# Performance work log

Measured on AMD Instinct MI355X. Metric: run time of the kernel, lower is better.

The kernel has to match this reference:

```python
import jax, jax.numpy as jnp
import numpy as np

NH = 2            # num heads
B = 2             # batch
CH = (64, 128, 256, 512)
HW = (128, 64, 32, 16)


def _mha(q, kv, w_in, b_in, w_out, b_out):
    # q, kv: [B, C, H, W] feature maps; seq layout (L, B, C) as in torch MHA (batch_first=False)
    Bq, C, H, W = q.shape
    L = H * W
    S = kv.shape[2] * kv.shape[3]
    qs = q.reshape(Bq, C, L).transpose(2, 0, 1)    # [L,B,C]
    ks = kv.reshape(Bq, C, S).transpose(2, 0, 1)   # [S,B,C]
    wq, wk, wv = jnp.split(w_in, 3, axis=0)        # torch in_proj_weight rows = [q; k; v]
    bq, bk, bv = jnp.split(b_in, 3)
    dh = C // NH
    qp = (qs @ wq.T + bq).reshape(L, Bq, NH, dh)
    kp = (ks @ wk.T + bk).reshape(S, Bq, NH, dh)
    vp = (ks @ wv.T + bv).reshape(S, Bq, NH, dh)
    scale = 1.0 / jnp.sqrt(jnp.asarray(dh, qp.dtype))
    scores = jnp.einsum('lbhd,sbhd->bhls', qp * scale, kp)  # [B,H,L,S]
    attn = jax.nn.softmax(scores, axis=-1)
    out = jnp.einsum('bhls,sbhd->lbhd', attn, vp).reshape(L, Bq, C)
    out = out @ w_out.T + b_out                    # out_proj
    return out.transpose(1, 2, 0).reshape(Bq, C, H, W)


def _level(fx1, fx2, fx3, w12, b12, ow12, ob12, w13, b13, ow13, ob13, sqw, sqb):
    att1 = _mha(fx1, fx2, w12, b12, ow12, ob12)
    att2 = _mha(fx1, fx3, w13, b13, ow13, ob13)
    cat = jnp.concatenate([fx1, att1, att2], axis=1)          # [B, 3C, H, W]
    return jnp.einsum('oc,bchw->bohw', sqw, cat) + sqb[None, :, None, None]  # 1x1 conv


def setup_inputs() -> dict:
    key = jax.random.key(0)
    ks = iter(jax.random.split(key, 64))
    d = {}
    for lvl in range(4):
        c, s = CH[lvl], HW[lvl]
        d[f'f1_{lvl}'] = jax.random.normal(next(ks), (B, c, s, s), jnp.float32)
    for lvl in range(1, 4):
        c, s = CH[lvl], HW[lvl]
        d[f'f2_{lvl}'] = jax.random.normal(next(ks), (B, c, s, s), jnp.float32)
        d[f'f3_{lvl}'] = jax.random.normal(next(ks), (B, c, s, s), jnp.float32)
    for i in (1, 2, 3):
        c = CH[i]
        sc = 1.0 / np.sqrt(c).astype(np.float32)
        for p in ('a12', 'a13'):
            d[f'{p}w{i}'] = jax.random.normal(next(ks), (3 * c, c), jnp.float32) * sc
            d[f'{p}b{i}'] = jnp.zeros((3 * c,), jnp.float32)
            d[f'{p}ow{i}'] = jax.random.normal(next(ks), (c, c), jnp.float32) * sc
            d[f'{p}ob{i}'] = jnp.zeros((c,), jnp.float32)
        d[f'sqw{i}'] = jax.random.normal(next(ks), (c, 3 * c), jnp.float32) * np.float32(1.0 / np.sqrt(3 * c))
        d[f'sqb{i}'] = jnp.zeros((c,), jnp.float32)
    return d


def reference(f1_0, f1_1, f1_2, f1_3, f2_1, f2_2, f2_3, f3_1, f3_2, f3_3,
              a12w1, a12b1, a12ow1, a12ob1, a13w1, a13b1, a13ow1, a13ob1, sqw1, sqb1,
              a12w2, a12b2, a12ow2, a12ob2, a13w2, a13b2, a13ow2, a13ob2, sqw2, sqb2,
              a12w3, a12b3, a12ow3, a12ob3, a13w3, a13b3, a13ow3, a13ob3, sqw3, sqb3):
    out0 = f1_0  # level 0 passes through untouched
    out1 = _level(f1_1, f2_1, f3_1, a12w1, a12b1, a12ow1, a12ob1, a13w1, a13b1, a13ow1, a13ob1, sqw1, sqb1)
    out2 = _level(f1_2, f2_2, f3_2, a12w2, a12b2, a12ow2, a12ob2, a13w2, a13b2, a13ow2, a13ob2, sqw2, sqb2)
    out3 = _level(f1_3, f2_3, f3_3, a12w3, a12b3, a12ow3, a12ob3, a13w3, a13b3, a13ow3, a13ob3, sqw3, sqb3)
    return (out0, out1, out2, out3)
```

## Files before the change

### kernel.cpp

```cpp
#include <hip/hip_runtime.h>
#include <hip/hip_bf16.h>
#include <math.h>

#define NHEADS 2

typedef unsigned short u16;
typedef __attribute__((ext_vector_type(8))) unsigned short u16x8;
typedef __attribute__((ext_vector_type(4))) unsigned short u16x4;
typedef __attribute__((ext_vector_type(8))) short short8;
typedef __attribute__((ext_vector_type(4))) short short4v;
typedef __attribute__((ext_vector_type(4))) float f32x4;

__device__ __forceinline__ u16 f2bf(float x) {
    __hip_bfloat16 h = __float2bfloat16(x);
    return __builtin_bit_cast(unsigned short, h);
}

__global__ __launch_bounds__(256) void gemm_qkv(
    const float* __restrict__ f1, const float* __restrict__ f2,
    const float* __restrict__ f3,
    const float* __restrict__ w12, const float* __restrict__ b12,
    const float* __restrict__ w13, const float* __restrict__ b13,
    u16* __restrict__ Qa, u16* __restrict__ Ka, u16* __restrict__ Va,
    u16* __restrict__ Qb, u16* __restrict__ Kb, u16* __restrict__ Vb,
    int M, int C, int L, int dh, float qscale, int gx, int perAtt)
{
    const int att = blockIdx.x / perAtt;
    const int r = blockIdx.x - att * perAtt;
    const int n0 = (r % gx) * 64;
    const int m0 = (r / gx) * 64;
    const int K = C;
    __shared__ __align__(16) u16 Xs[64][72];
    __shared__ __align__(16) u16 Ws[64][72];
    const int tid = threadIdx.x;
    const int wid = tid >> 6, lane = tid & 63;
    const int lo = lane & 15, hi = lane >> 4;
    const int wm = wid >> 1, wn = wid & 1;

    const float* __restrict__ Xf = (n0 < C) ? f1 : (att ? f3 : f2);
    const float* __restrict__ W = att ? w13 : w12;
    const float* __restrict__ bias = att ? b13 : b12;
    const int bb = m0 / L;
    const int l0 = m0 - bb * L;

    f32x4 acc[2][2];
    #pragma unroll
    for (int i = 0; i < 2; ++i)
        #pragma unroll
        for (int j = 0; j < 2; ++j)
            #pragma unroll
            for (int rr = 0; rr < 4; ++rr) acc[i][j][rr] = 0.f;

    f32x4 xregf[4];
    f32x4 wreg[4];
    const int kx = tid >> 4;
    const int lc = tid & 15;

    auto load_x = [&](int k0) {
        #pragma unroll
        for (int i = 0; i < 4; ++i)
            xregf[i] = *(const f32x4*)&Xf[((size_t)(bb * C) + k0 + kx + 16 * i) * L + l0 + lc * 4];
    };
    auto store_x = [&]() {
        #pragma unroll
        for (int i = 0; i < 4; ++i)
            #pragma unroll
            for (int j = 0; j < 4; ++j)
                Xs[lc * 4 + j][kx + 16 * i] = f2bf(xregf[i][j]);
    };
    auto load_w = [&](int k0) {
        #pragma unroll
        for (int p = 0; p < 4; ++p) {
            int c = tid + p * 256;
            int row = c >> 4, kc = c & 15;
            wreg[p] = *(const f32x4*)&W[(size_t)(n0 + row) * K + k0 + kc * 4];
        }
    };

    load_x(0);
    load_w(0);
    const int ns = K / 64;
    for (int s = 0; s < ns; ++s) {
        __syncthreads();
        store_x();
        #pragma unroll
        for (int p = 0; p < 4; ++p) {
            int c = tid + p * 256;
            int row = c >> 4, kc = c & 15;
            u16x4 cv = {f2bf(wreg[p][0]), f2bf(wreg[p][1]),
                        f2bf(wreg[p][2]), f2bf(wreg[p][3])};
            *(u16x4*)&Ws[row][kc * 4] = cv;
        }
        __syncthreads();
        if (s + 1 < ns) { load_x((s + 1) * 64); load_w((s + 1) * 64); }
        #pragma unroll
        for (int kk = 0; kk < 2; ++kk) {
            short8 wf0 = *(const short8*)&Ws[wn * 32 + lo][kk * 32 + hi * 8];
            short8 wf1 = *(const short8*)&Ws[wn * 32 + 16 + lo][kk * 32 + hi * 8];
            short8 xf0 = *(const short8*)&Xs[wm * 32 + lo][kk * 32 + hi * 8];
            short8 xf1 = *(const short8*)&Xs[wm * 32 + 16 + lo][kk * 32 + hi * 8];
            acc[0][0] = __builtin_amdgcn_mfma_f32_16x16x32_bf16(wf0, xf0, acc[0][0], 0, 0, 0);
            acc[0][1] = __builtin_amdgcn_mfma_f32_16x16x32_bf16(wf1, xf0, acc[0][1], 0, 0, 0);
            acc[1][0] = __builtin_amdgcn_mfma_f32_16x16x32_bf16(wf0, xf1, acc[1][0], 0, 0, 0);
            acc[1][1] = __builtin_amdgcn_mfma_f32_16x16x32_bf16(wf1, xf1, acc[1][1], 0, 0, 0);
        }
    }

    #pragma unroll
    for (int nt = 0; nt < 2; ++nt) {
        const int nb = n0 + wn * 32 + nt * 16 + hi * 4;
        const float b0 = bias[nb + 0], b1 = bias[nb + 1];
        const float b2 = bias[nb + 2], b3 = bias[nb + 3];
        const int which = nb / C;
        const int co = nb - which * C;
        const int h = co / dh;
        const int dd = co - h * dh;
        u16* dst = (which == 0) ? (att ? Qb : Qa)
                 : (which == 1) ? (att ? Kb : Ka) : (att ? Vb : Va);
        const float sc = (which == 0) ? qscale : 1.0f;
        #pragma unroll
        for (int mt = 0; mt < 2; ++mt) {
            int m = m0 + wm * 32 + mt * 16 + lo;
            int b_ = m / L; int l = m - b_ * L;
            u16x4 pk = {f2bf((acc[mt][nt][0] + b0) * sc),
                        f2bf((acc[mt][nt][1] + b1) * sc),
                        f2bf((acc[mt][nt][2] + b2) * sc),
                        f2bf((acc[mt][nt][3] + b3) * sc)};
            *(u16x4*)&dst[((size_t)(b_ * NHEADS + h) * L + l) * dh + dd] = pk;
        }
    }
}

__global__ __launch_bounds__(256) void prep_w(
    const float* __restrict__ s1, const float* __restrict__ oa1,
    const float* __restrict__ ob1, float* __restrict__ w1,
    const float* __restrict__ s2, const float* __restrict__ oa2,
    const float* __restrict__ ob2, float* __restrict__ w2,
    const float* __restrict__ s3, const float* __restrict__ oa3,
    const float* __restrict__ ob3, float* __restrict__ w3)
{
    int bid = blockIdx.x;
    int C; const float *sqw, *owa, *owb; float* wp;
    if (bid < 12)      { C = 128; sqw = s1; owa = oa1; owb = ob1; wp = w1; }
    else if (bid < 60) { bid -= 12; C = 256; sqw = s2; owa = oa2; owb = ob2; wp = w2; }
    else               { bid -= 60; C = 512; sqw = s3; owa = oa3; owb = ob3; wp = w3; }
    const int K3 = 3 * C;
    const int gxw = K3 / 64;
    const int n0 = (bid / gxw) * 64;
    const int kc0 = (bid % gxw) * 64;
    const int tid = threadIdx.x;

    if (kc0 < C) {
        for (int p = tid; p < 64 * 64; p += 256) {
            int i = p >> 6, j = p & 63;
            wp[(size_t)(n0 + i) * K3 + kc0 + j] = sqw[(size_t)(n0 + i) * K3 + kc0 + j];
        }
        return;
    }
    const int which = kc0 / C;
    const int kp0 = kc0 - which * C;
    const float* __restrict__ ow = (which == 1) ? owa : owb;

    __shared__ __align__(16) u16 As[64][72];
    __shared__ __align__(16) u16 Bs[64][72];
    const int wid = tid >> 6, lane = tid & 63;
    const int lo = lane & 15, hi = lane >> 4;
    const int wm = wid >> 1, wn = wid & 1;

    f32x4 acc[2][2];
    #pragma unroll
    for (int i = 0; i < 2; ++i)
        #pragma unroll
        for (int j = 0; j < 2; ++j)
            #pragma unroll
            for (int rr = 0; rr < 4; ++rr) acc[i][j][rr] = 0.f;

    for (int ct = 0; ct < C / 64; ++ct) {
        __syncthreads();
        for (int p = tid; p < 64 * 64; p += 256) {
            int i = p >> 6, j = p & 63;
            As[i][j] = f2bf(sqw[(size_t)(n0 + i) * K3 + which * C + ct * 64 + j]);
            Bs[j][i] = f2bf(ow[(size_t)(ct * 64 + i) * C + kp0 + j]);
        }
        __syncthreads();
        #pragma unroll
        for (int kk = 0; kk < 2; ++kk) {
            short8 wf0 = *(const short8*)&As[wn * 32 + lo][kk * 32 + hi * 8];
            short8 wf1 = *(const short8*)&As[wn * 32 + 16 + lo][kk * 32 + hi * 8];
            short8 xf0 = *(const short8*)&Bs[wm * 32 + lo][kk * 32 + hi * 8];
            short8 xf1 = *(const short8*)&Bs[wm * 32 + 16 + lo][kk * 32 + hi * 8];
            acc[0][0] = __builtin_amdgcn_mfma_f32_16x16x32_bf16(wf0, xf0, acc[0][0], 0, 0, 0);
            acc[0][1] = __builtin_amdgcn_mfma_f32_16x16x32_bf16(wf1, xf0, acc[0][1], 0, 0, 0);
            acc[1][0] = __builtin_amdgcn_mfma_f32_16x16x32_bf16(wf0, xf1, acc[1][0], 0, 0, 0);
            acc[1][1] = __builtin_amdgcn_mfma_f32_16x16x32_bf16(wf1, xf1, acc[1][1], 0, 0, 0);
        }
    }
    #pragma unroll
    for (int nt = 0; nt < 2; ++nt) {
        const int nb = n0 + wn * 32 + nt * 16 + hi * 4;
        #pragma unroll
        for (int mt = 0; mt < 2; ++mt) {
            const int col = kc0 + wm * 32 + mt * 16 + lo;
            #pragma unroll
            for (int rr = 0; rr < 4; ++rr)
                wp[(size_t)(nb + rr) * K3 + col] = acc[mt][nt][rr];
        }
    }
}

__global__ __launch_bounds__(256) void prep_b(
    const float* __restrict__ s1, const float* __restrict__ oba1,
    const float* __restrict__ obb1, const float* __restrict__ sqb1, float* __restrict__ b1,
    const float* __restrict__ s2, const float* __restrict__ oba2,
    const float* __restrict__ obb2, const float* __restrict__ sqb2, float* __restrict__ b2,
    const float* __restrict__ s3, const float* __restrict__ oba3,
    const float* __restrict__ obb3, const float* __restrict__ sqb3, float* __restrict__ b3)
{
    int bid = blockIdx.x;
    int C, n;
    const float *sqw, *oba, *obb, *sqb; float* bp;
    if (bid < 128)      { C = 128; n = bid;       sqw = s1; oba = oba1; obb = obb1; sqb = sqb1; bp = b1; }
    else if (bid < 384) { C = 256; n = bid - 128; sqw = s2; oba = oba2; obb = obb2; sqb = sqb2; bp = b2; }
    else                { C = 512; n = bid - 384; sqw = s3; oba = oba3; obb = obb3; sqb = sqb3; bp = b3; }

    const float* row = sqw + (size_t)n * 3 * C;
    float s = 0.f;
    for (int c = threadIdx.x; c < C; c += 256)
        s += row[C + c] * oba[c] + row[2 * C + c] * obb[c];
    #pragma unroll
    for (int off = 1; off < 64; off <<= 1)
        s += __shfl_xor(s, off);
    __shared__ float ws[4];
    const int wv = threadIdx.x >> 6;
    if ((threadIdx.x & 63) == 0) ws[wv] = s;
    __syncthreads();
    if (threadIdx.x == 0)
        bp[n] = sqb[n] + ws[0] + ws[1] + ws[2] + ws[3];
}

__global__ __launch_bounds__(256) void gemm_squeeze(
    const float* __restrict__ F1, const u16* __restrict__ X1,
    const u16* __restrict__ X2,
    const float* __restrict__ W, const float* __restrict__ bias,
    float* __restrict__ out, int M, int C, int L)
{
    const int n0 = blockIdx.x * 64;
    const int m0 = blockIdx.y * 64;
    const int K = 3 * C;
    __shared__ __align__(16) u16 Xs[64][72];
    __shared__ __align__(16) u16 Ws[64][72];
    const int tid = threadIdx.x;
    const int wid = tid >> 6, lane = tid & 63;
    const int lo = lane & 15, hi = lane >> 4;
    const int wm = wid >> 1, wn = wid & 1;
    const int bb = m0 / L;
    const int l0 = m0 - bb * L;

    f32x4 acc[2][2];
    #pragma unroll
    for (int i = 0; i < 2; ++i)
        #pragma unroll
        for (int j = 0; j < 2; ++j)
            #pragma unroll
            for (int rr = 0; rr < 4; ++rr) acc[i][j][rr] = 0.f;

    f32x4 xregf[4];
    u16x8 xreg[2];
    f32x4 wreg[4];
    const int kx = tid >> 4;
    const int lc = tid & 15;

    auto load_x = [&](int k0) {
        if (k0 < C) {
            #pragma unroll
            for (int i = 0; i < 4; ++i)
                xregf[i] = *(const f32x4*)&F1[((size_t)(bb * C) + k0 + kx + 16 * i) * L + l0 + lc * 4];
        } else {
            const u16* src = (k0 < 2 * C) ? X1 : X2;
            int kl = k0 - ((k0 < 2 * C) ? C : 2 * C);
            #pragma unroll
            for (int p = 0; p < 2; ++p) {
                int c = tid + p * 256;
                int row = c >> 3, kc = c & 7;
                xreg[p] = *(const u16x8*)&src[(size_t)(m0 + row) * C + kl + kc * 8];
            }
        }
    };
    auto store_x = [&](int k0) {
        if (k0 < C) {
            #pragma unroll
            for (int i = 0; i < 4; ++i)
                #pragma unroll
                for (int j = 0; j < 4; ++j)
                    Xs[lc * 4 + j][kx + 16 * i] = f2bf(xregf[i][j]);
        } else {
            #pragma unroll
            for (int p = 0; p < 2; ++p) {
                int c = tid + p * 256;
                int row = c >> 3, kc = c & 7;
                *(u16x8*)&Xs[row][kc * 8] = xreg[p];
            }
        }
    };
    auto load_w = [&](int k0) {
        #pragma unroll
        for (int p = 0; p < 4; ++p) {
            int c = tid + p * 256;
            int row = c >> 4, kc = c & 15;
            wreg[p] = *(const f32x4*)&W[(size_t)(n0 + row) * K + k0 + kc * 4];
        }
    };

    load_x(0);
    load_w(0);
    const int ns = K / 64;
    for (int s = 0; s < ns; ++s) {
        __syncthreads();
        store_x(s * 64);
        #pragma unroll
        for (int p = 0; p < 4; ++p) {
            int c = tid + p * 256;
            int row = c >> 4, kc = c & 15;
            u16x4 cv = {f2bf(wreg[p][0]), f2bf(wreg[p][1]),
                        f2bf(wreg[p][2]), f2bf(wreg[p][3])};
            *(u16x4*)&Ws[row][kc * 4] = cv;
        }
        __syncthreads();
        if (s + 1 < ns) { load_x((s + 1) * 64); load_w((s + 1) * 64); }
        #pragma unroll
        for (int kk = 0; kk < 2; ++kk) {
            short8 wf0 = *(const short8*)&Ws[wn * 32 + lo][kk * 32 + hi * 8];
            short8 wf1 = *(const short8*)&Ws[wn * 32 + 16 + lo][kk * 32 + hi * 8];
            short8 xf0 = *(const short8*)&Xs[wm * 32 + lo][kk * 32 + hi * 8];
            short8 xf1 = *(const short8*)&Xs[wm * 32 + 16 + lo][kk * 32 + hi * 8];
            acc[0][0] = __builtin_amdgcn_mfma_f32_16x16x32_bf16(wf0, xf0, acc[0][0], 0, 0, 0);
            acc[0][1] = __builtin_amdgcn_mfma_f32_16x16x32_bf16(wf1, xf0, acc[0][1], 0, 0, 0);
            acc[1][0] = __builtin_amdgcn_mfma_f32_16x16x32_bf16(wf0, xf1, acc[1][0], 0, 0, 0);
            acc[1][1] = __builtin_amdgcn_mfma_f32_16x16x32_bf16(wf1, xf1, acc[1][1], 0, 0, 0);
        }
    }

    #pragma unroll
    for (int nt = 0; nt < 2; ++nt) {
        const int nb = n0 + wn * 32 + nt * 16 + hi * 4;
        const float b0 = bias[nb + 0], b1 = bias[nb + 1];
        const float b2 = bias[nb + 2], b3 = bias[nb + 3];
        #pragma unroll
        for (int mt = 0; mt < 2; ++mt) {
            int m = m0 + wm * 32 + mt * 16 + lo;
            int b_ = m / L; int l = m - b_ * L;
            out[((size_t)(b_ * C + nb + 0)) * L + l] = acc[mt][nt][0] + b0;
            out[((size_t)(b_ * C + nb + 1)) * L + l] = acc[mt][nt][1] + b1;
            out[((size_t)(b_ * C + nb + 2)) * L + l] = acc[mt][nt][2] + b2;
            out[((size_t)(b_ * C + nb + 3)) * L + l] = acc[mt][nt][3] + b3;
        }
    }
}

template <int DH, int NPAR, int NQS>
__global__ __launch_bounds__(128 * NPAR) void flash_split(
    const u16* __restrict__ Q1, const u16* __restrict__ K1,
    const u16* __restrict__ V1, u16* __restrict__ O1,
    const u16* __restrict__ Q2, const u16* __restrict__ K2,
    const u16* __restrict__ V2, u16* __restrict__ O2, int L, int S)
{
    constexpr int KB = 64;
    constexpr int QW = 16 * NQS;
    constexpr int QB = 2 * QW;
    constexpr int NKK = DH / 32;
    constexpr int NNT = DH / 16;
    constexpr int DG = DH / 8;
    constexpr int SLOTS = DG / 8;
    constexpr int SZ_VT = 2 * NPAR * DH * KB * 2;
    constexpr int MST = DH + 4;
    constexpr int P = NPAR - 1;

    __shared__ __align__(16) char smem[SZ_VT];
    u16 (*Vt)[NPAR][DH][KB] = (u16 (*)[NPAR][DH][KB])smem;
    float* MrgAcc = (float*)smem;
    float* MrgML  = (float*)(smem + (size_t)2 * P * QW * MST * 4);

    const int nQT = L / QB;
    const int perAtt = 2 * NHEADS * nQT;
    const int att = blockIdx.x / perAtt;
    const int rem = blockIdx.x - att * perAtt;
    const int qt = rem % nQT;
    const int bh = rem / nQT;
    const u16* __restrict__ Q = att ? Q2 : Q1;
    const u16* __restrict__ K = att ? K2 : K1;
    const u16* __restrict__ V = att ? V2 : V1;
    u16* __restrict__ O = att ? O2 : O1;

    const int tid = threadIdx.x;
    const int w = tid >> 6;
    const int lane = tid & 63;
    const int lo = lane & 15, hi = lane >> 4;
    const int qg = w & 1, par = w >> 1;
    const int q0 = qt * QB + qg * QW;

    short8 qf[NQS][NKK];
    #pragma unroll
    for (int qs = 0; qs < NQS; ++qs)
        #pragma unroll
        for (int kk = 0; kk < NKK; ++kk)
            qf[qs][kk] = *(const short8*)&Q[((size_t)bh * L + q0 + qs * 16 + lo) * DH + kk * 32 + hi * 8];

    f32x4 acc[NQS][NNT];
    #pragma unroll
    for (int qs = 0; qs < NQS; ++qs)
        #pragma unroll
        for (int nt = 0; nt < NNT; ++nt)
            #pragma unroll
            for (int r = 0; r < 4; ++r) acc[qs][nt][r] = 0.f;
    float m_i[NQS], l_i[NQS];
    #pragma unroll
    for (int qs = 0; qs < NQS; ++qs) { m_i[qs] = -1e30f; l_i[qs] = 0.f; }

    const u16* Kbase = K + (size_t)bh * S * DH;
    const u16* Vbase = V + (size_t)bh * S * DH;

    short8 kf[4][NKK];
    auto load_kf = [&](int r) {
        const u16* Kt = Kbase + (size_t)(NPAR * r + par) * KB * DH;
        #pragma unroll
        for (int st = 0; st < 4; ++st)
            #pragma unroll
            for (int kk = 0; kk < NKK; ++kk)
                kf[st][kk] = *(const short8*)&Kt[(size_t)(st * 16 + lo) * DH + kk * 32 + hi * 8];
    };

    const int pt = tid >> 7;
    const int u = tid & 127;
    int dV0[SLOTS], sV0[SLOTS];
    #pragma unroll
    for (int z = 0; z < SLOTS; ++z) {
        int e = u + z * 128;
        dV0[z] = (e % DG) * 8;
        sV0[z] = (e / DG) * 4;
    }

    u16x8 vreg[SLOTS][4];

    auto loadslots = [&](int r) {
        const u16* Vp = Vbase + (size_t)(NPAR * r + pt) * KB * DH;
        #pragma unroll
        for (int z = 0; z < SLOTS; ++z)
            #pragma unroll
            for (int si = 0; si < 4; ++si)
                vreg[z][si] = *(const u16x8*)&Vp[(size_t)(sV0[z] + si) * DH + dV0[z]];
    };
    auto writeslots = [&](int buf) {
        #pragma unroll
        for (int z = 0; z < SLOTS; ++z)
            #pragma unroll
            for (int j = 0; j < 8; ++j) {
                int d = dV0[z] + j;
                int g = ((d >> 3) ^ d) & 7;
                int scol = (sV0[z] & 7) | ((((sV0[z] >> 3) ^ g) & 7) << 3);
                u16x4 wj = {vreg[z][0][j], vreg[z][1][j], vreg[z][2][j], vreg[z][3][j]};
                *(u16x4*)&Vt[buf][pt][d][scol] = wj;
            }
    };

    const int NR = S / (KB * NPAR);

    load_kf(0);
    loadslots(0);
    writeslots(0);
    __syncthreads();
    if (1 < NR) loadslots(1);

    for (int r = 0; r < NR; ++r) {
        const int cur = r & 1;

        f32x4 sacc[4][NQS];
        #pragma unroll
        for (int st = 0; st < 4; ++st)
            #pragma unroll
            for (int qs = 0; qs < NQS; ++qs)
                #pragma unroll
                for (int rr = 0; rr < 4; ++rr) sacc[st][qs][rr] = 0.f;
        #pragma unroll
        for (int st = 0; st < 4; ++st) {
            #pragma unroll
            for (int kk = 0; kk < NKK; ++kk) {
                #pragma unroll
                for (int qs = 0; qs < NQS; ++qs)
                    sacc[st][qs] = __builtin_amdgcn_mfma_f32_16x16x32_bf16(
                        kf[st][kk], qf[qs][kk], sacc[st][qs], 0, 0, 0);
            }
        }

        if (r + 1 < NR) load_kf(r + 1);

        float mn[NQS], ts[NQS];
        #pragma unroll
        for (int qs = 0; qs < NQS; ++qs) {
            float tm = -1e30f;
            #pragma unroll
            for (int st = 0; st < 4; ++st)
                #pragma unroll
                for (int rr = 0; rr < 4; ++rr) tm = fmaxf(tm, sacc[st][qs][rr]);
            tm = fmaxf(tm, __shfl_xor(tm, 16));
            tm = fmaxf(tm, __shfl_xor(tm, 32));
            const bool grow = __any(tm > m_i[qs] + 8.0f);
            mn[qs] = grow ? fmaxf(m_i[qs], tm) : m_i[qs];
            ts[qs] = 0.f;
            if (grow) {
                float alpha = __builtin_amdgcn_exp2f(m_i[qs] - mn[qs]);
                m_i[qs] = mn[qs];
                l_i[qs] *= alpha;
                float ar[4];
                #pragma unroll
                for (int rr = 0; rr < 4; ++rr) ar[rr] = __shfl(alpha, hi * 4 + rr);
                #pragma unroll
                for (int nt = 0; nt < NNT; ++nt)
                    #pragma unroll
                    for (int rr = 0; rr < 4; ++rr) acc[qs][nt][rr] *= ar[rr];
            }
        }

        if (r + 1 < NR) writeslots(cur ^ 1);

        __builtin_amdgcn_s_setprio(1);
        #pragma unroll
        for (int st = 0; st < 4; ++st) {
            short4v pa_[NQS];
            #pragma unroll
            for (int qs = 0; qs < NQS; ++qs) {
                float p0 = __builtin_amdgcn_exp2f(sacc[st][qs][0] - mn[qs]);
                float p1 = __builtin_amdgcn_exp2f(sacc[st][qs][1] - mn[qs]);
                float p2 = __builtin_amdgcn_exp2f(sacc[st][qs][2] - mn[qs]);
                float p3 = __builtin_amdgcn_exp2f(sacc[st][qs][3] - mn[qs]);
                ts[qs] += (p0 + p1) + (p2 + p3);
                short4v pk = {(short)f2bf(p0), (short)f2bf(p1),
                              (short)f2bf(p2), (short)f2bf(p3)};
                pa_[qs] = pk;
            }
            const int s0 = st * 16 + hi * 4;
            #pragma unroll
            for (int nt = 0; nt < NNT; ++nt) {
                int d = nt * 16 + lo;
                int g = ((d >> 3) ^ d) & 7;
                int scol = (s0 & 7) | ((((s0 >> 3) ^ g) & 7) << 3);
                short4v vb = *(const short4v*)&Vt[cur][par][d][scol];
                #pragma unroll
                for (int qs = 0; qs < NQS; ++qs)
                    acc[qs][nt] = __builtin_amdgcn_mfma_f32_16x16x16bf16_1k(
                        pa_[qs], vb, acc[qs][nt], 0, 0, 0);
            }
        }
        __builtin_amdgcn_s_setprio(0);

        #pragma unroll
        for (int qs = 0; qs < NQS; ++qs) {
            float t2 = ts[qs];
            t2 += __shfl_xor(t2, 16);
            t2 += __shfl_xor(t2, 32);
            l_i[qs] += t2;
        }

        __syncthreads();
        if (r + 2 < NR) loadslots(r + 2);
    }

    const int b_ = bh / NHEADS, h_ = bh % NHEADS;
    if (par != 0) {
        const int mi = qg * P + par - 1;
        float* ma = MrgAcc + (size_t)mi * QW * MST;
        #pragma unroll
        for (int qs = 0; qs < NQS; ++qs) {
            #pragma unroll
            for (int nt = 0; nt < NNT; ++nt)
                #pragma unroll
                for (int rr = 0; rr < 4; ++rr)
                    ma[(size_t)(qs * 16 + hi * 4 + rr) * MST + nt * 16 + lo] = acc[qs][nt][rr];
            if (hi == 0) {
                MrgML[(mi * 2 + 0) * QW + qs * 16 + lo] = m_i[qs];
                MrgML[(mi * 2 + 1) * QW + qs * 16 + lo] = l_i[qs];
            }
        }
    }
    __syncthreads();
    if (par == 0) {
        #pragma unroll
        for (int qs = 0; qs < NQS; ++qs) {
            float mp[P > 0 ? P : 1], lp[P > 0 ? P : 1];
            float mt = m_i[qs];
            #pragma unroll
            for (int p = 0; p < P; ++p) {
                mp[p] = MrgML[((qg * P + p) * 2 + 0) * QW + qs * 16 + lo];
                lp[p] = MrgML[((qg * P + p) * 2 + 1) * QW + qs * 16 + lo];
                mt = fmaxf(mt, mp[p]);
            }
            float c0 = __builtin_amdgcn_exp2f(m_i[qs] - mt);
            float lt = c0 * l_i[qs];
            float cp[P > 0 ? P : 1];
            #pragma unroll
            for (int p = 0; p < P; ++p) {
                cp[p] = __builtin_amdgcn_exp2f(mp[p] - mt);
                lt += cp[p] * lp[p];
            }
            float linv = 1.0f / lt;
            c0 *= linv;
            #pragma unroll
            for (int p = 0; p < P; ++p) cp[p] *= linv;
            float c0r[4], cpr[P > 0 ? P : 1][4];
            #pragma unroll
            for (int rr = 0; rr < 4; ++rr) {
                c0r[rr] = __shfl(c0, hi * 4 + rr);
                #pragma unroll
                for (int p = 0; p < P; ++p) cpr[p][rr] = __shfl(cp[p], hi * 4 + rr);
            }
            #pragma unroll
            for (int nt = 0; nt < NNT; ++nt)
                #pragma unroll
                for (int rr = 0; rr < 4; ++rr) {
                    int q = qs * 16 + hi * 4 + rr;
                    float ov = acc[qs][nt][rr] * c0r[rr];
                    #pragma unroll
                    for (int p = 0; p < P; ++p)
                        ov += MrgAcc[((size_t)(qg * P + p) * QW + q) * MST + nt * 16 + lo] * cpr[p][rr];
                    O[(((size_t)b_ * L + q0 + q) * NHEADS + h_) * DH + nt * 16 + lo] = f2bf(ov);
                }
        }
    }
}

template <int DH, int NQS, int PRE>
__global__ __launch_bounds__(128) void flash_mfma(
    const u16* __restrict__ Q1, const u16* __restrict__ K1,
    const u16* __restrict__ V1, u16* __restrict__ O1,
    const u16* __restrict__ Q2, const u16* __restrict__ K2,
    const u16* __restrict__ V2, u16* __restrict__ O2, int L, int S)
{
    constexpr int KB = 64;
    constexpr int QW = NQS * 16;
    constexpr int QB = 2 * QW;
    constexpr int DH8 = DH / 8;
    constexpr int KC = (KB * DH8) / 128;
    constexpr int VU = (16 * DH8) / 128;
    constexpr int NKK = DH / 32;
    constexpr int NNT = DH / 16;

    __shared__ __align__(16) u16 Ks[KB][DH + 8];
    __shared__ __align__(16) u16 Vt[DH][KB];

    const int nQT = L / QB;
    const int perAtt = 2 * NHEADS * nQT;
    const int att = blockIdx.x / perAtt;
    const int rem = blockIdx.x - att * perAtt;
    const int qt = rem % nQT;
    const int bh = rem / nQT;
    const u16* __restrict__ Q = att ? Q2 : Q1;
    const u16* __restrict__ K = att ? K2 : K1;
    const u16* __restrict__ V = att ? V2 : V1;
    u16* __restrict__ O = att ? O2 : O1;

    const int tid = threadIdx.x;
    const int wv = tid >> 6;
    const int lane = tid & 63;
    const int lo = lane & 15;
    const int hi = lane >> 4;
    const int q0 = qt * QB + wv * QW;

    short8 qf[NQS][NKK];
    #pragma unroll
    for (int qs = 0; qs < NQS; ++qs)
        #pragma unroll
        for (int kk = 0; kk < NKK; ++kk)
            qf[qs][kk] = *(const short8*)&Q[((size_t)bh * L + q0 + qs * 16 + lo) * DH + kk * 32 + hi * 8];

    f32x4 acc[NQS][NNT];
    #pragma unroll
    for (int qs = 0; qs < NQS; ++qs)
        #pragma unroll
        for (int nt = 0; nt < NNT; ++nt)
            #pragma unroll
            for (int r = 0; r < 4; ++r) acc[qs][nt][r] = 0.f;
    float m_i[NQS], l_i[NQS];
    #pragma unroll
    for (int qs = 0; qs < NQS; ++qs) { m_i[qs] = -1e30f; l_i[qs] = 0.f; }

    const int NT = S / KB;
    u16x8 kreg[PRE ? KC : 1];
    u16x8 vreg[PRE ? VU : 1][4];

    const u16* Kbase = K + (size_t)bh * S * DH;
    const u16* Vbase = V + (size_t)bh * S * DH;

    auto vwrite = [&](int d, int s0, u16x4 wj) {
        int g = ((d >> 3) ^ d) & 7;
        int scol = (s0 & 7) | ((((s0 >> 3) ^ g) & 7) << 3);
        *(u16x4*)&Vt[d][scol] = wj;
    };

    if (PRE) {
        #pragma unroll
        for (int i = 0; i < KC; ++i) {
            int idx = tid + i * 128;
            kreg[i] = *(const u16x8*)&Kbase[(size_t)(idx / DH8) * DH + (idx % DH8) * 8];
        }
        #pragma unroll
        for (int u = 0; u < VU; ++u) {
            int uu = tid + u * 128;
            int d0 = (uu % DH8) * 8, s0 = (uu / DH8) * 4;
            #pragma unroll
            for (int si = 0; si < 4; ++si)
                vreg[u][si] = *(const u16x8*)&Vbase[(size_t)(s0 + si) * DH + d0];
        }
    }

    for (int t = 0; t < NT; ++t) {
        __syncthreads();
        if (PRE) {
            #pragma unroll
            for (int i = 0; i < KC; ++i) {
                int idx = tid + i * 128;
                *(u16x8*)&Ks[idx / DH8][(idx % DH8) * 8] = kreg[i];
            }
            #pragma unroll
            for (int u = 0; u < VU; ++u) {
                int uu = tid + u * 128;
                int d0 = (uu % DH8) * 8, s0 = (uu / DH8) * 4;
                #pragma unroll
                for (int j = 0; j < 8; ++j) {
                    u16x4 wj = {vreg[u][0][j], vreg[u][1][j], vreg[u][2][j], vreg[u][3][j]};
                    vwrite(d0 + j, s0, wj);
                }
            }
        } else {
            const u16* Kp = Kbase + (size_t)t * KB * DH;
            const u16* Vp = Vbase + (size_t)t * KB * DH;
            #pragma unroll
            for (int i = 0; i < KC; ++i) {
                int idx = tid + i * 128;
                *(u16x8*)&Ks[idx / DH8][(idx % DH8) * 8] =
                    *(const u16x8*)&Kp[(size_t)(idx / DH8) * DH + (idx % DH8) * 8];
            }
            #pragma unroll
            for (int u = 0; u < VU; ++u) {
                int uu = tid + u * 128;
                int d0 = (uu % DH8) * 8, s0 = (uu / DH8) * 4;
                u16x8 v0 = *(const u16x8*)&Vp[(size_t)(s0 + 0) * DH + d0];
                u16x8 v1 = *(const u16x8*)&Vp[(size_t)(s0 + 1) * DH + d0];
                u16x8 v2 = *(const u16x8*)&Vp[(size_t)(s0 + 2) * DH + d0];
                u16x8 v3 = *(const u16x8*)&Vp[(size_t)(s0 + 3) * DH + d0];
                #pragma unroll
                for (int j = 0; j < 8; ++j) {
                    u16x4 wj = {v0[j], v1[j], v2[j], v3[j]};
                    vwrite(d0 + j, s0, wj);
                }
            }
        }
        __syncthreads();

        if (PRE && t + 1 < NT) {
            const u16* Kp = Kbase + (size_t)(t + 1) * KB * DH;
            const u16* Vp = Vbase + (size_t)(t + 1) * KB * DH;
            #pragma unroll
            for (int i = 0; i < KC; ++i) {
                int idx = tid + i * 128;
                kreg[i] = *(const u16x8*)&Kp[(size_t)(idx / DH8) * DH + (idx % DH8) * 8];
            }
            #pragma unroll
            for (int u = 0; u < VU; ++u) {
                int uu = tid + u * 128;
                int d0 = (uu % DH8) * 8, s0 = (uu / DH8) * 4;
                #pragma unroll
                for (int si = 0; si < 4; ++si)
                    vreg[u][si] = *(const u16x8*)&Vp[(size_t)(s0 + si) * DH + d0];
            }
        }

        f32x4 sacc[4][NQS];
        #pragma unroll
        for (int st = 0; st < 4; ++st)
            #pragma unroll
            for (int qs = 0; qs < NQS; ++qs)
                #pragma unroll
                for (int r = 0; r < 4; ++r) sacc[st][qs][r] = 0.f;
        #pragma unroll
        for (int st = 0; st < 4; ++st) {
            #pragma unroll
            for (int kk = 0; kk < NKK; ++kk) {
                short8 a = *(const short8*)&Ks[st * 16 + lo][kk * 32 + hi * 8];
                #pragma unroll
                for (int qs = 0; qs < NQS; ++qs)
                    sacc[st][qs] = __builtin_amdgcn_mfma_f32_16x16x32_bf16(
                        a, qf[qs][kk], sacc[st][qs], 0, 0, 0);
            }
        }

        float mn[NQS], ts[NQS];
        #pragma unroll
        for (int qs = 0; qs < NQS; ++qs) {
            float tm = -1e30f;
            #pragma unroll
            for (int st = 0; st < 4; ++st)
                #pragma unroll
                for (int r = 0; r < 4; ++r) tm = fmaxf(tm, sacc[st][qs][r]);
            tm = fmaxf(tm, __shfl_xor(tm, 16));
            tm = fmaxf(tm, __shfl_xor(tm, 32));
            const bool grow = __any(tm > m_i[qs] + 8.0f);
            mn[qs] = grow ? fmaxf(m_i[qs], tm) : m_i[qs];
            ts[qs] = 0.f;
            if (grow) {
                float alpha = __builtin_amdgcn_exp2f(m_i[qs] - mn[qs]);
                m_i[qs] = mn[qs];
                l_i[qs] *= alpha;
                float ar[4];
                #pragma unroll
                for (int r = 0; r < 4; ++r) ar[r] = __shfl(alpha, hi * 4 + r);
                #pragma unroll
                for (int nt = 0; nt < NNT; ++nt)
                    #pragma unroll
                    for (int r = 0; r < 4; ++r) acc[qs][nt][r] *= ar[r];
            }
        }

        #pragma unroll
        for (int st = 0; st < 4; ++st) {
            short4v pa_[NQS];
            #pragma unroll
            for (int qs = 0; qs < NQS; ++qs) {
                float p0 = __builtin_amdgcn_exp2f(sacc[st][qs][0] - mn[qs]);
                float p1 = __builtin_amdgcn_exp2f(sacc[st][qs][1] - mn[qs]);
                float p2 = __builtin_amdgcn_exp2f(sacc[st][qs][2] - mn[qs]);
                float p3 = __builtin_amdgcn_exp2f(sacc[st][qs][3] - mn[qs]);
                ts[qs] += (p0 + p1) + (p2 + p3);
                short4v pk = {(short)f2bf(p0), (short)f2bf(p1),
                              (short)f2bf(p2), (short)f2bf(p3)};
                pa_[qs] = pk;
            }
            const int s0 = st * 16 + hi * 4;
            #pragma unroll
            for (int nt = 0; nt < NNT; ++nt) {
                int d = nt * 16 + lo;
                int g = ((d >> 3) ^ d) & 7;
                int scol = (s0 & 7) | ((((s0 >> 3) ^ g) & 7) << 3);
                short4v vb = *(const short4v*)&Vt[d][scol];
                #pragma unroll
                for (int qs = 0; qs < NQS; ++qs)
                    acc[qs][nt] = __builtin_amdgcn_mfma_f32_16x16x16bf16_1k(
                        pa_[qs], vb, acc[qs][nt], 0, 0, 0);
            }
        }

        #pragma unroll
        for (int qs = 0; qs < NQS; ++qs) {
            float t2 = ts[qs];
            t2 += __shfl_xor(t2, 16);
            t2 += __shfl_xor(t2, 32);
            l_i[qs] += t2;
        }
    }

    const int b_ = bh / NHEADS, h_ = bh % NHEADS;
    #pragma unroll
    for (int qs = 0; qs < NQS; ++qs) {
        float inv = 1.0f / l_i[qs];
        float ir[4];
        #pragma unroll
        for (int r = 0; r < 4; ++r) ir[r] = __shfl(inv, hi * 4 + r);
        #pragma unroll
        for (int nt = 0; nt < NNT; ++nt)
            #pragma unroll
            for (int r = 0; r < 4; ++r) {
                int l = q0 + qs * 16 + hi * 4 + r;
                O[(((size_t)b_ * L + l) * NHEADS + h_) * DH + nt * 16 + lo] =
                    f2bf(acc[qs][nt][r] * ir[r]);
            }
    }
}


extern "C" void kernel_launch(void* const* d_in, const int* in_sizes, int n_in,
                              void* d_out, int out_size, void* d_ws, size_t ws_size,
                              hipStream_t stream)
{
    static const int CHs[4] = {64, 128, 256, 512};
    static const int HWs[4] = {128, 64, 32, 16};

    const float* f1[4] = {(const float*)d_in[0], (const float*)d_in[1],
                          (const float*)d_in[2], (const float*)d_in[3]};
    const float* f2[4] = {nullptr, (const float*)d_in[4], (const float*)d_in[6],
                          (const float*)d_in[8]};
    const float* f3[4] = {nullptr, (const float*)d_in[5], (const float*)d_in[7],
                          (const float*)d_in[9]};

    size_t out0_elems = (size_t)in_sizes[0];
    hipMemcpyAsync(d_out, d_in[0], out0_elems * sizeof(float),
                   hipMemcpyDeviceToDevice, stream);

    const size_t SL = (size_t)2 * 4096 * 128;
    u16* wsu = (u16*)d_ws;
    u16* Qa  = wsu + 0 * SL;
    u16* Ka  = wsu + 1 * SL;
    u16* Va  = wsu + 2 * SL;
    u16* Qb  = wsu + 3 * SL;
    u16* Kb  = wsu + 4 * SL;
    u16* Vb  = wsu + 5 * SL;
    u16* Ana = wsu + 6 * SL;
    u16* Anb = wsu + 7 * SL;
    float* wp1 = (float*)(wsu + 8 * SL);
    float* wp2 = wp1 + (size_t)128 * 384;
    float* wp3 = wp2 + (size_t)256 * 768;
    float* bp1 = wp3 + (size_t)512 * 1536;
    float* bp2 = bp1 + 512;
    float* bp3 = bp2 + 512;

    const float* SQW[3]; const float* OWA[3]; const float* OWB[3];
    const float* OBA[3]; const float* OBB[3]; const float* SQB[3];
    for (int l = 0; l < 3; ++l) {
        const int bi = 10 + l * 10;
        OWA[l] = (const float*)d_in[bi + 2];
        OBA[l] = (const float*)d_in[bi + 3];
        OWB[l] = (const float*)d_in[bi + 6];
        OBB[l] = (const float*)d_in[bi + 7];
        SQW[l] = (const float*)d_in[bi + 8];
        SQB[l] = (const float*)d_in[bi + 9];
    }

    prep_w<<<252, 256, 0, stream>>>(SQW[0], OWA[0], OWB[0], wp1,
                                    SQW[1], OWA[1], OWB[1], wp2,
                                    SQW[2], OWA[2], OWB[2], wp3);
    prep_b<<<896, 256, 0, stream>>>(SQW[0], OBA[0], OBB[0], SQB[0], bp1,
                                    SQW[1], OBA[1], OBB[1], SQB[1], bp2,
                                    SQW[2], OBA[2], OBB[2], SQB[2], bp3);

    const float LOG2E = 1.44269504088896340736f;

    size_t outOff = out0_elems;
    for (int lvl = 1; lvl <= 3; ++lvl) {
        const int C = CHs[lvl];
        const int Hs = HWs[lvl];
        const int L = Hs * Hs;
        const int dh = C / NHEADS;
        const int M = 2 * L;
        const float qscale = LOG2E / sqrtf((float)dh);
        const int bi = 10 + (lvl - 1) * 10;
        const float* a12w = (const float*)d_in[bi + 0];
        const float* a12b = (const float*)d_in[bi + 1];
        const float* a13w = (const float*)d_in[bi + 4];
        const float* a13b = (const float*)d_in[bi + 5];
        float* wp = (lvl == 1) ? wp1 : (lvl == 2) ? wp2 : wp3;
        float* bp = (lvl == 1) ? bp1 : (lvl == 2) ? bp2 : bp3;

        const int gx = 3 * C / 64;
        const int perAtt = gx * (M / 64);
        gemm_qkv<<<2 * perAtt, 256, 0, stream>>>(
            f1[lvl], f2[lvl], f3[lvl], a12w, a12b, a13w, a13b,
            Qa, Ka, Va, Qb, Kb, Vb, M, C, L, dh, qscale, gx, perAtt);

        if (dh == 64)
            flash_split<64, 4, 2><<<2 * (2 * NHEADS) * (L / 64), 512, 0, stream>>>(
                Qa, Ka, Va, Ana, Qb, Kb, Vb, Anb, L, L);
        else if (dh == 128)
            flash_split<128, 2, 1><<<2 * (2 * NHEADS) * (L / 32), 256, 0, stream>>>(
                Qa, Ka, Va, Ana, Qb, Kb, Vb, Anb, L, L);
        else
            flash_mfma<256, 1, 0><<<2 * (2 * NHEADS) * (L / 32), 128, 0, stream>>>(
                Qa, Ka, Va, Ana, Qb, Kb, Vb, Anb, L, L);

        dim3 gsq(C / 64, M / 64);
        gemm_squeeze<<<gsq, 256, 0, stream>>>(f1[lvl], Ana, Anb, wp, bp,
                                              (float*)d_out + outOff, M, C, L);
        outOff += (size_t)2 * C * L;
    }
}
```

Baseline: 280.6 us.

## Merge per-level QKV, prep, and squeeze launches into batched multi-level kernels

Gives each level its own Q/K/V/attention workspace slices so the three levels no longer share buffers. That allows all QKV projections plus the weight and bias prep to run in one launch, and all three squeeze GEMMs in another. This cuts the launch count, removes serialization between levels, and fills the GPU better on the small levels. The cost is a larger workspace footprint and branchy dispatch inside the merged kernels, which may raise register pressure.

```diff
diff --git a/kernel.cpp b/kernel.cpp
--- a/kernel.cpp
+++ b/kernel.cpp
@@ -16,30 +16,40 @@
     return __builtin_bit_cast(unsigned short, h);
 }
 
-__global__ __launch_bounds__(256) void gemm_qkv(
-    const float* __restrict__ f1, const float* __restrict__ f2,
-    const float* __restrict__ f3,
-    const float* __restrict__ w12, const float* __restrict__ b12,
-    const float* __restrict__ w13, const float* __restrict__ b13,
-    u16* __restrict__ Qa, u16* __restrict__ Ka, u16* __restrict__ Va,
-    u16* __restrict__ Qb, u16* __restrict__ Kb, u16* __restrict__ Vb,
-    int M, int C, int L, int dh, float qscale, int gx, int perAtt)
+struct QkvLvl {
+    const float *f1, *f2, *f3;
+    const float *w12, *b12, *w13, *b13;
+    u16 *Qa, *Ka, *Va, *Qb, *Kb, *Vb;
+    int C, L, dh, gx, perAtt;
+    float qscale;
+};
+struct PrepArgs {
+    const float *sqw[3], *owa[3], *owb[3], *oba[3], *obb[3], *sqb[3];
+    float *wp[3], *bp[3];
+};
+struct SqLvl {
+    const float* F1; const u16 *X1, *X2;
+    const float *W, *bias; float* out;
+    int M, C, L, gx, nblk;
+};
+
+__device__ __forceinline__ void qkv_dev(const QkvLvl& A, int lbid,
+                                        u16 (*Xs)[72], u16 (*Ws)[72])
 {
-    const int att = blockIdx.x / perAtt;
-    const int r = blockIdx.x - att * perAtt;
-    const int n0 = (r % gx) * 64;
-    const int m0 = (r / gx) * 64;
+    const int att = lbid / A.perAtt;
+    const int r = lbid - att * A.perAtt;
+    const int n0 = (r % A.gx) * 64;
+    const int m0 = (r / A.gx) * 64;
+    const int C = A.C, L = A.L, dh = A.dh;
     const int K = C;
-    __shared__ __align__(16) u16 Xs[64][72];
-    __shared__ __align__(16) u16 Ws[64][72];
     const int tid = threadIdx.x;
     const int wid = tid >> 6, lane = tid & 63;
     const int lo = lane & 15, hi = lane >> 4;
     const int wm = wid >> 1, wn = wid & 1;
 
-    const float* __restrict__ Xf = (n0 < C) ? f1 : (att ? f3 : f2);
-    const float* __restrict__ W = att ? w13 : w12;
-    const float* __restrict__ bias = att ? b13 : b12;
+    const float* __restrict__ Xf = (n0 < C) ? A.f1 : (att ? A.f3 : A.f2);
+    const float* __restrict__ W = att ? A.w13 : A.w12;
+    const float* __restrict__ bias = att ? A.b13 : A.b12;
     const int bb = m0 / L;
     const int l0 = m0 - bb * L;
 
@@ -115,9 +125,9 @@
         const int co = nb - which * C;
         const int h = co / dh;
         const int dd = co - h * dh;
-        u16* dst = (which == 0) ? (att ? Qb : Qa)
-                 : (which == 1) ? (att ? Kb : Ka) : (att ? Vb : Va);
-        const float sc = (which == 0) ? qscale : 1.0f;
+        u16* dst = (which == 0) ? (att ? A.Qb : A.Qa)
+                 : (which == 1) ? (att ? A.Kb : A.Ka) : (att ? A.Vb : A.Va);
+        const float sc = (which == 0) ? A.qscale : 1.0f;
         #pragma unroll
         for (int mt = 0; mt < 2; ++mt) {
             int m = m0 + wm * 32 + mt * 16 + lo;
@@ -131,19 +141,17 @@
     }
 }
 
-__global__ __launch_bounds__(256) void prep_w(
-    const float* __restrict__ s1, const float* __restrict__ oa1,
-    const float* __restrict__ ob1, float* __restrict__ w1,
-    const float* __restrict__ s2, const float* __restrict__ oa2,
-    const float* __restrict__ ob2, float* __restrict__ w2,
-    const float* __restrict__ s3, const float* __restrict__ oa3,
-    const float* __restrict__ ob3, float* __restrict__ w3)
+__device__ __forceinline__ void prepw_dev(const PrepArgs& P, int bid,
+                                          u16 (*As)[72], u16 (*Bs)[72])
 {
-    int bid = blockIdx.x;
-    int C; const float *sqw, *owa, *owb; float* wp;
-    if (bid < 12)      { C = 128; sqw = s1; owa = oa1; owb = ob1; wp = w1; }
-    else if (bid < 60) { bid -= 12; C = 256; sqw = s2; owa = oa2; owb = ob2; wp = w2; }
-    else               { bid -= 60; C = 512; sqw = s3; owa = oa3; owb = ob3; wp = w3; }
+    int C; int lv;
+    if (bid < 12)      { C = 128; lv = 0; }
+    else if (bid < 60) { bid -= 12; C = 256; lv = 1; }
+    else               { bid -= 60; C = 512; lv = 2; }
+    const float* sqw = P.sqw[lv];
+    const float* owa = P.owa[lv];
+    const float* owb = P.owb[lv];
+    float* wp = P.wp[lv];
     const int K3 = 3 * C;
     const int gxw = K3 / 64;
     const int n0 = (bid / gxw) * 64;
@@ -161,8 +169,6 @@
     const int kp0 = kc0 - which * C;
     const float* __restrict__ ow = (which == 1) ? owa : owb;
 
-    __shared__ __align__(16) u16 As[64][72];
-    __shared__ __align__(16) u16 Bs[64][72];
     const int wid = tid >> 6, lane = tid & 63;
     const int lo = lane & 15, hi = lane >> 4;
     const int wm = wid >> 1, wn = wid & 1;
@@ -208,20 +214,17 @@
     }
 }
 
-__global__ __launch_bounds__(256) void prep_b(
-    const float* __restrict__ s1, const float* __restrict__ oba1,
-    const float* __restrict__ obb1, const float* __restrict__ sqb1, float* __restrict__ b1,
-    const float* __restrict__ s2, const float* __restrict__ oba2,
-    const float* __restrict__ obb2, const float* __restrict__ sqb2, float* __restrict__ b2,
-    const float* __restrict__ s3, const float* __restrict__ oba3,
-    const float* __restrict__ obb3, const float* __restrict__ sqb3, float* __restrict__ b3)
+__device__ __forceinline__ void prepb_dev(const PrepArgs& P, int bid, float* ws4)
 {
-    int bid = blockIdx.x;
-    int C, n;
-    const float *sqw, *oba, *obb, *sqb; float* bp;
-    if (bid < 128)      { C = 128; n = bid;       sqw = s1; oba = oba1; obb = obb1; sqb = sqb1; bp = b1; }
-    else if (bid < 384) { C = 256; n = bid - 128; sqw = s2; oba = oba2; obb = obb2; sqb = sqb2; bp = b2; }
-    else                { C = 512; n = bid - 384; sqw = s3; oba = oba3; obb = obb3; sqb = sqb3; bp = b3; }
+    int C, n, lv;
+    if (bid < 128)      { C = 128; n = bid;       lv = 0; }
+    else if (bid < 384) { C = 256; n = bid - 128; lv = 1; }
+    else                { C = 512; n = bid - 384; lv = 2; }
+    const float* sqw = P.sqw[lv];
+    const float* oba = P.oba[lv];
+    const float* obb = P.obb[lv];
+    const float* sqb = P.sqb[lv];
+    float* bp = P.bp[lv];
 
     const float* row = sqw + (size_t)n * 3 * C;
     float s = 0.f;
@@ -230,25 +233,39 @@
     #pragma unroll
     for (int off = 1; off < 64; off <<= 1)
         s += __shfl_xor(s, off);
-    __shared__ float ws[4];
     const int wv = threadIdx.x >> 6;
-    if ((threadIdx.x & 63) == 0) ws[wv] = s;
+    if ((threadIdx.x & 63) == 0) ws4[wv] = s;
     __syncthreads();
     if (threadIdx.x == 0)
-        bp[n] = sqb[n] + ws[0] + ws[1] + ws[2] + ws[3];
+        bp[n] = sqb[n] + ws4[0] + ws4[1] + ws4[2] + ws4[3];
 }
 
-__global__ __launch_bounds__(256) void gemm_squeeze(
-    const float* __restrict__ F1, const u16* __restrict__ X1,
-    const u16* __restrict__ X2,
-    const float* __restrict__ W, const float* __restrict__ bias,
-    float* __restrict__ out, int M, int C, int L)
+__global__ __launch_bounds__(256) void stage1(
+    QkvLvl a0, QkvLvl a1, QkvLvl a2, PrepArgs P,
+    int n0q, int n1q, int n2q, int npw)
 {
-    const int n0 = blockIdx.x * 64;
-    const int m0 = blockIdx.y * 64;
-    const int K = 3 * C;
     __shared__ __align__(16) u16 Xs[64][72];
     __shared__ __align__(16) u16 Ws[64][72];
+    __shared__ float ws4[4];
+    int bid = blockIdx.x;
+    if (bid < n0q)                { qkv_dev(a0, bid, Xs, Ws); return; }
+    bid -= n0q;
+    if (bid < n1q)                { qkv_dev(a1, bid, Xs, Ws); return; }
+    bid -= n1q;
+    if (bid < n2q)                { qkv_dev(a2, bid, Xs, Ws); return; }
+    bid -= n2q;
+    if (bid < npw)                { prepw_dev(P, bid, Xs, Ws); return; }
+    bid -= npw;
+    prepb_dev(P, bid, ws4);
+}
+
+__device__ __forceinline__ void squeeze_dev(const SqLvl& A, int idx,
+                                            u16 (*Xs)[72], u16 (*Ws)[72])
+{
+    const int n0 = (idx % A.gx) * 64;
+    const int m0 = (idx / A.gx) * 64;
+    const int C = A.C, L = A.L;
+    const int K = 3 * C;
     const int tid = threadIdx.x;
     const int wid = tid >> 6, lane = tid & 63;
     const int lo = lane & 15, hi = lane >> 4;
@@ -274,9 +291,9 @@
         if (k0 < C) {
             #pragma unroll
             for (int i = 0; i < 4; ++i)
-                xregf[i] = *(const f32x4*)&F1[((size_t)(bb * C) + k0 + kx + 16 * i) * L + l0 + lc * 4];
+                xregf[i] = *(const f32x4*)&A.F1[((size_t)(bb * C) + k0 + kx + 16 * i) * L + l0 + lc * 4];
         } else {
-            const u16* src = (k0 < 2 * C) ? X1 : X2;
+            const u16* src = (k0 < 2 * C) ? A.X1 : A.X2;
             int kl = k0 - ((k0 < 2 * C) ? C : 2 * C);
             #pragma unroll
             for (int p = 0; p < 2; ++p) {
@@ -307,7 +324,7 @@
         for (int p = 0; p < 4; ++p) {
             int c = tid + p * 256;
             int row = c >> 4, kc = c & 15;
-            wreg[p] = *(const f32x4*)&W[(size_t)(n0 + row) * K + k0 + kc * 4];
+            wreg[p] = *(const f32x4*)&A.W[(size_t)(n0 + row) * K + k0 + kc * 4];
         }
     };
 
@@ -343,18 +360,30 @@
     #pragma unroll
     for (int nt = 0; nt < 2; ++nt) {
         const int nb = n0 + wn * 32 + nt * 16 + hi * 4;
-        const float b0 = bias[nb + 0], b1 = bias[nb + 1];
-        const float b2 = bias[nb + 2], b3 = bias[nb + 3];
+        const float b0 = A.bias[nb + 0], b1 = A.bias[nb + 1];
+        const float b2 = A.bias[nb + 2], b3 = A.bias[nb + 3];
         #pragma unroll
         for (int mt = 0; mt < 2; ++mt) {
             int m = m0 + wm * 32 + mt * 16 + lo;
             int b_ = m / L; int l = m - b_ * L;
-            out[((size_t)(b_ * C + nb + 0)) * L + l] = acc[mt][nt][0] + b0;
-            out[((size_t)(b_ * C + nb + 1)) * L + l] = acc[mt][nt][1] + b1;
-            out[((size_t)(b_ * C + nb + 2)) * L + l] = acc[mt][nt][2] + b2;
-            out[((size_t)(b_ * C + nb + 3)) * L + l] = acc[mt][nt][3] + b3;
-        }
-    }
+            A.out[((size_t)(b_ * C + nb + 0)) * L + l] = acc[mt][nt][0] + b0;
+            A.out[((size_t)(b_ * C + nb + 1)) * L + l] = acc[mt][nt][1] + b1;
+            A.out[((size_t)(b_ * C + nb + 2)) * L + l] = acc[mt][nt][2] + b2;
+            A.out[((size_t)(b_ * C + nb + 3)) * L + l] = acc[mt][nt][3] + b3;
+        }
+    }
+}
+
+__global__ __launch_bounds__(256) void squeeze_all(SqLvl s0, SqLvl s1, SqLvl s2)
+{
+    __shared__ __align__(16) u16 Xs[64][72];
+    __shared__ __align__(16) u16 Ws[64][72];
+    int bid = blockIdx.x;
+    if (bid < s0.nblk)      { squeeze_dev(s0, bid, Xs, Ws); return; }
+    bid -= s0.nblk;
+    if (bid < s1.nblk)      { squeeze_dev(s1, bid, Xs, Ws); return; }
+    bid -= s1.nblk;
+    squeeze_dev(s2, bid, Xs, Ws);
 }
 
 template <int DH, int NPAR, int NQS>
@@ -893,79 +922,90 @@
     hipMemcpyAsync(d_out, d_in[0], out0_elems * sizeof(float),
                    hipMemcpyDeviceToDevice, stream);
 
-    const size_t SL = (size_t)2 * 4096 * 128;
-    u16* wsu = (u16*)d_ws;
-    u16* Qa  = wsu + 0 * SL;
-    u16* Ka  = wsu + 1 * SL;
-    u16* Va  = wsu + 2 * SL;
-    u16* Qb  = wsu + 3 * SL;
-    u16* Kb  = wsu + 4 * SL;
-    u16* Vb  = wsu + 5 * SL;
-    u16* Ana = wsu + 6 * SL;
-    u16* Anb = wsu + 7 * SL;
-    float* wp1 = (float*)(wsu + 8 * SL);
+    const size_t QE[3] = {(size_t)2 * NHEADS * 4096 * 64,
+                          (size_t)2 * NHEADS * 1024 * 128,
+                          (size_t)2 * NHEADS * 256 * 256};
+
+    u16* p = (u16*)d_ws;
+    u16 *Qa[3], *Ka[3], *Va[3], *Qb[3], *Kb[3], *Vb[3], *Ana[3], *Anb[3];
+    for (int l = 0; l < 3; ++l) {
+        Qa[l] = p; p += QE[l];  Ka[l] = p; p += QE[l];  Va[l] = p; p += QE[l];
+        Qb[l] = p; p += QE[l];  Kb[l] = p; p += QE[l];  Vb[l] = p; p += QE[l];
+        Ana[l] = p; p += QE[l]; Anb[l] = p; p += QE[l];
+    }
+    float* wp1 = (float*)p;
     float* wp2 = wp1 + (size_t)128 * 384;
     float* wp3 = wp2 + (size_t)256 * 768;
     float* bp1 = wp3 + (size_t)512 * 1536;
     float* bp2 = bp1 + 512;
     float* bp3 = bp2 + 512;
 
-    const float* SQW[3]; const float* OWA[3]; const float* OWB[3];
-    const float* OBA[3]; const float* OBB[3]; const float* SQB[3];
+    const float LOG2E = 1.44269504088896340736f;
+
+    QkvLvl qa[3];
+    PrepArgs P;
+    int nq[3];
     for (int l = 0; l < 3; ++l) {
+        const int lvl = l + 1;
+        const int C = CHs[lvl], Hs = HWs[lvl];
+        const int L = Hs * Hs, dh = C / NHEADS, M = 2 * L;
         const int bi = 10 + l * 10;
-        OWA[l] = (const float*)d_in[bi + 2];
-        OBA[l] = (const float*)d_in[bi + 3];
-        OWB[l] = (const float*)d_in[bi + 6];
-        OBB[l] = (const float*)d_in[bi + 7];
-        SQW[l] = (const float*)d_in[bi + 8];
-        SQB[l] = (const float*)d_in[bi + 9];
-    }
-
-    prep_w<<<252, 256, 0, stream>>>(SQW[0], OWA[0], OWB[0], wp1,
-                                    SQW[1], OWA[1], OWB[1], wp2,
-                                    SQW[2], OWA[2], OWB[2], wp3);
-    prep_b<<<896, 256, 0, stream>>>(SQW[0], OBA[0], OBB[0], SQB[0], bp1,
-                                    SQW[1], OBA[1], OBB[1], SQB[1], bp2,
-                                    SQW[2], OBA[2], OBB[2], SQB[2], bp3);
-
-    const float LOG2E = 1.44269504088896340736f;
-
+        qa[l].f1 = f1[lvl]; qa[l].f2 = f2[lvl]; qa[l].f3 = f3[lvl];
+        qa[l].w12 = (const float*)d_in[bi + 0];
+        qa[l].b12 = (const float*)d_in[bi + 1];
+        qa[l].w13 = (const float*)d_in[bi + 4];
+        qa[l].b13 = (const float*)d_in[bi + 5];
+        qa[l].Qa = Qa[l]; qa[l].Ka = Ka[l]; qa[l].Va = Va[l];
+        qa[l].Qb = Qb[l]; qa[l].Kb = Kb[l]; qa[l].Vb = Vb[l];
+        qa[l].C = C; qa[l].L = L; qa[l].dh = dh;
+        qa[l].gx = 3 * C / 64;
+        qa[l].perAtt = qa[l].gx * (M / 64);
+        qa[l].qscale = LOG2E / sqrtf((float)dh);
+        nq[l] = 2 * qa[l].perAtt;
+        P.owa[l] = (const float*)d_in[bi + 2];
+        P.oba[l] = (const float*)d_in[bi + 3];
+        P.owb[l] = (const float*)d_in[bi + 6];
+        P.obb[l] = (const float*)d_in[bi + 7];
+        P.sqw[l] = (const float*)d_in[bi + 8];
+        P.sqb[l] = (const float*)d_in[bi + 9];
+    }
+    P.wp[0] = wp1; P.wp[1] = wp2; P.wp[2] = wp3;
+    P.bp[0] = bp1; P.bp[1] = bp2; P.bp[2] = bp3;
+
+    const int NPW = 252, NPB = 896;
+    const int totalS1 = nq[0] + nq[1] + nq[2] + NPW + NPB;
+
+    stage1<<<totalS1, 256, 0, stream>>>(qa[0], qa[1], qa[2], P,
+                                        nq[0], nq[1], nq[2], NPW);
+
+    {
+        const int L1 = 4096;
+        flash_split<64, 4, 2><<<2 * (2 * NHEADS) * (L1 / 64), 512, 0, stream>>>(
+            Qa[0], Ka[0], Va[0], Ana[0], Qb[0], Kb[0], Vb[0], Anb[0], L1, L1);
+        const int L2 = 1024;
+        flash_split<128, 2, 1><<<2 * (2 * NHEADS) * (L2 / 32), 256, 0, stream>>>(
+            Qa[1], Ka[1], Va[1], Ana[1], Qb[1], Kb[1], Vb[1], Anb[1], L2, L2);
+        const int L3 = 256;
+        flash_mfma<256, 1, 0><<<2 * (2 * NHEADS) * (L3 / 32), 128, 0, stream>>>(
+            Qa[2], Ka[2], Va[2], Ana[2], Qb[2], Kb[2], Vb[2], Anb[2], L3, L3);
+    }
+
+    SqLvl sq[3];
     size_t outOff = out0_elems;
-    for (int lvl = 1; lvl <= 3; ++lvl) {
-        const int C = CHs[lvl];
-        const int Hs = HWs[lvl];
-        const int L = Hs * Hs;
-        const int dh = C / NHEADS;
-        const int M = 2 * L;
-        const float qscale = LOG2E / sqrtf((float)dh);
-        const int bi = 10 + (lvl - 1) * 10;
-        const float* a12w = (const float*)d_in[bi + 0];
-        const float* a12b = (const float*)d_in[bi + 1];
-        const float* a13w = (const float*)d_in[bi + 4];
-        const float* a13b = (const float*)d_in[bi + 5];
-        float* wp = (lvl == 1) ? wp1 : (lvl == 2) ? wp2 : wp3;
-        float* bp = (lvl == 1) ? bp1 : (lvl == 2) ? bp2 : bp3;
-
-        const int gx = 3 * C / 64;
-        const int perAtt = gx * (M / 64);
-        gemm_qkv<<<2 * perAtt, 256, 0, stream>>>(
-            f1[lvl], f2[lvl], f3[lvl], a12w, a12b, a13w, a13b,
-            Qa, Ka, Va, Qb, Kb, Vb, M, C, L, dh, qscale, gx, perAtt);
-
-        if (dh == 64)
-            flash_split<64, 4, 2><<<2 * (2 * NHEADS) * (L / 64), 512, 0, stream>>>(
-                Qa, Ka, Va, Ana, Qb, Kb, Vb, Anb, L, L);
-        else if (dh == 128)
-            flash_split<128, 2, 1><<<2 * (2 * NHEADS) * (L / 32), 256, 0, stream>>>(
-                Qa, Ka, Va, Ana, Qb, Kb, Vb, Anb, L, L);
-        else
-            flash_mfma<256, 1, 0><<<2 * (2 * NHEADS) * (L / 32), 128, 0, stream>>>(
-                Qa, Ka, Va, Ana, Qb, Kb, Vb, Anb, L, L);
-
-        dim3 gsq(C / 64, M / 64);
-        gemm_squeeze<<<gsq, 256, 0, stream>>>(f1[lvl], Ana, Anb, wp, bp,
-                                              (float*)d_out + outOff, M, C, L);
+    for (int l = 0; l < 3; ++l) {
+        const int lvl = l + 1;
+        const int C = CHs[lvl], Hs = HWs[lvl];
+        const int L = Hs * Hs, M = 2 * L;
+        sq[l].F1 = f1[lvl];
+        sq[l].X1 = Ana[l]; sq[l].X2 = Anb[l];
+        sq[l].W = (l == 0) ? wp1 : (l == 1) ? wp2 : wp3;
+        sq[l].bias = (l == 0) ? bp1 : (l == 1) ? bp2 : bp3;
+        sq[l].out = (float*)d_out + outOff;
+        sq[l].M = M; sq[l].C = C; sq[l].L = L;
+        sq[l].gx = C / 64;
+        sq[l].nblk = sq[l].gx * (M / 64);
         outOff += (size_t)2 * C * L;
     }
+    squeeze_all<<<sq[0].nblk + sq[1].nblk + sq[2].nblk, 256, 0, stream>>>(
+        sq[0], sq[1], sq[2]);
 }
```

Measured after the change: 349.1 us. 24.4% more time.
